# Kernel tuning notes

Measured on AMD Instinct MI355X. Metric: run time of the kernel, lower is better.

The kernel has to match this reference:

```python
import jax, jax.numpy as jnp
import numpy as np

D_MODEL = 2048
NUM_HEADS = 16
HEAD_DIM = D_MODEL // NUM_HEADS


def setup_inputs() -> dict:
    key = jax.random.key(0)
    ks = jax.random.split(key, 9)
    B, S, D = 2, 2048, D_MODEL
    scale = 1.0 / np.sqrt(D)
    x = jax.random.normal(ks[0], (B, S, D), dtype=jnp.float32)
    # torch nn.Linear weights are [out, in]; y = x @ W.T + b
    wq = jax.random.normal(ks[1], (D, D), dtype=jnp.float32) * scale
    wk = jax.random.normal(ks[2], (D, D), dtype=jnp.float32) * scale
    wv = jax.random.normal(ks[3], (D, D), dtype=jnp.float32) * scale
    wo = jax.random.normal(ks[4], (D, D), dtype=jnp.float32) * scale
    bq = jax.random.normal(ks[5], (D,), dtype=jnp.float32) * scale
    bk = jax.random.normal(ks[6], (D,), dtype=jnp.float32) * scale
    bv = jax.random.normal(ks[7], (D,), dtype=jnp.float32) * scale
    bo = jax.random.normal(ks[8], (D,), dtype=jnp.float32) * scale
    return {"x": x, "wq": wq, "bq": bq, "wk": wk, "bk": bk,
            "wv": wv, "bv": bv, "wo": wo, "bo": bo}


def reference(x, wq, bq, wk, bk, wv, bv, wo, bo):
    B, S, D = x.shape
    H, Dh = NUM_HEADS, HEAD_DIM
    # projections (torch Linear: x @ W.T + b), reshape to [B, H, S, Dh]
    q = (x @ wq.T + bq).reshape(B, S, H, Dh).transpose(0, 2, 1, 3)
    k = (x @ wk.T + bk).reshape(B, S, H, Dh).transpose(0, 2, 1, 3)
    v = (x @ wv.T + bv).reshape(B, S, H, Dh).transpose(0, 2, 1, 3)
    scores = jnp.einsum("bhqd,bhkd->bhqk", q, k) / jnp.sqrt(jnp.float32(Dh))
    attn = jax.nn.softmax(scores, axis=-1)
    out = jnp.einsum("bhqk,bhkd->bhqd", attn, v)  # [B, H, S, Dh]
    out = out.transpose(0, 2, 1, 3).reshape(B, S, D)
    return out @ wo.T + bo
```

## Files before the change

kernel.cpp:

```cpp
#include <hip/hip_runtime.h>

#define DEV __device__ __forceinline__

typedef __attribute__((ext_vector_type(8))) short bf16x8;
typedef __attribute__((ext_vector_type(4))) float f32x4;

constexpr int D_MODEL = 2048;
constexpr int NHEAD = 16;
constexpr int DH = 128;
constexpr int SS = 2048;
constexpr int KK = 2048;

DEV unsigned short f2bf(float f) {
  unsigned int u = __builtin_bit_cast(unsigned int, f);
  u = (u + 0x7fff + ((u >> 16) & 1)) >> 16;
  return (unsigned short)u;
}

DEV void async16(const void* g, void* l) {
  __builtin_amdgcn_global_load_lds(
      (const __attribute__((address_space(1))) unsigned int*)g,
      (__attribute__((address_space(3))) unsigned int*)l, 16, 0, 0);
}

DEV f32x4 mfma16(bf16x8 a, bf16x8 b, f32x4 c) {
  return __builtin_amdgcn_mfma_f32_16x16x32_bf16(a, b, c, 0, 0, 0);
}

__global__ __launch_bounds__(256) void cast_all(
    const float* __restrict__ x, const float* __restrict__ wq,
    const float* __restrict__ wk, const float* __restrict__ wv,
    const float* __restrict__ wo, unsigned short* __restrict__ xb,
    unsigned short* __restrict__ wb) {
  long i4 = ((long)blockIdx.x * 256 + threadIdx.x) * 4;
  const float* src;
  unsigned short* dst;
  long off;
  if (i4 < 8388608) {
    src = x; dst = xb; off = i4;
  } else {
    long j = i4 - 8388608;
    int seg = (int)(j >> 22);
    off = j & 4194303;
    src = (seg == 0) ? wq : (seg == 1) ? wk : (seg == 2) ? wv : wo;
    dst = wb + ((long)seg << 22);
  }
  float4 v = *(const float4*)(src + off);
  ushort4 u;
  u.x = f2bf(v.x); u.y = f2bf(v.y); u.z = f2bf(v.z); u.w = f2bf(v.w);
  *(ushort4*)(dst + off) = u;
}

template <int MODE>
__global__ __launch_bounds__(256, 2) void gemm_bt(
    const unsigned short* __restrict__ A, const unsigned short* __restrict__ W,
    const float* __restrict__ b0, const float* __restrict__ b1,
    const float* __restrict__ b2, unsigned short* __restrict__ oq,
    unsigned short* __restrict__ ok, unsigned short* __restrict__ ov,
    float* __restrict__ of) {
  __shared__ unsigned short lA[128 * 32];
  __shared__ unsigned short lB[128 * 32];
  const int t = threadIdx.x;
  const int lane = t & 63, wid = t >> 6;
  const int m0 = blockIdx.y * 128, n0 = blockIdx.x * 128;
  const int srow = t >> 2, scol = (t & 3) * 8;
  const unsigned short* ga = A + (long)(m0 + srow) * KK + scol;
  const unsigned short* gw = W + (long)(n0 + srow) * KK + scol;
  const int i16 = lane & 15, g4 = lane >> 4;
  const int wr = wid >> 1, wc = wid & 1;
  f32x4 acc[4][4] = {};
  for (int k0 = 0; k0 < KK; k0 += 32) {
    async16(ga + k0, &lA[wid * 512]);
    async16(ga + 64 * KK + k0, &lA[2048 + wid * 512]);
    async16(gw + k0, &lB[wid * 512]);
    async16(gw + 64 * KK + k0, &lB[2048 + wid * 512]);
    __syncthreads();
    bf16x8 af[4], bfr[4];
#pragma unroll
    for (int i = 0; i < 4; i++)
      af[i] = *(const bf16x8*)&lA[(wr * 64 + i * 16 + i16) * 32 + g4 * 8];
#pragma unroll
    for (int j = 0; j < 4; j++)
      bfr[j] = *(const bf16x8*)&lB[(wc * 64 + j * 16 + i16) * 32 + g4 * 8];
#pragma unroll
    for (int i = 0; i < 4; i++)
#pragma unroll
      for (int j = 0; j < 4; j++) acc[i][j] = mfma16(af[i], bfr[j], acc[i][j]);
    __syncthreads();
  }
#pragma unroll
  for (int i = 0; i < 4; i++) {
#pragma unroll
    for (int j = 0; j < 4; j++) {
      const int ng = n0 + wc * 64 + j * 16 + i16;
#pragma unroll
      for (int r = 0; r < 4; r++) {
        const int mg = m0 + wr * 64 + i * 16 + g4 * 4 + r;
        float v = acc[i][j][r];
        if (MODE == 1) {
          v += b0[ng];
          of[(long)mg * D_MODEL + ng] = v;
        } else {
          const int seg = ng >> 11, n = ng & 2047;
          const int h = n >> 7, d = n & 127;
          const int b_ = mg >> 11, s_ = mg & 2047;
          const long bh = b_ * NHEAD + h;
          if (seg == 0) {
            v = (v + b0[n]) * 0.08838834764831845f;
            oq[(bh * SS + s_) * DH + d] = f2bf(v);
          } else if (seg == 1) {
            v += b1[n];
            ok[(bh * SS + s_) * DH + d] = f2bf(v);
          } else {
            v += b2[n];
            ov[(bh * DH + d) * SS + s_] = f2bf(v);
          }
        }
      }
    }
  }
}

__global__ __launch_bounds__(256, 2) void attn_fwd(
    const unsigned short* __restrict__ Q, const unsigned short* __restrict__ Kb,
    const unsigned short* __restrict__ Vt, unsigned short* __restrict__ Ob) {
  __shared__ unsigned short lK[64 * 128];
  __shared__ unsigned short lV[128 * 64];
  __shared__ unsigned short lP[4][16 * 64];
  const int t = threadIdx.x, lane = t & 63, wid = t >> 6;
  const int i16 = lane & 15, g4 = lane >> 4;
  const int qt = blockIdx.x, bh = blockIdx.y;
  const long qrow = (long)bh * SS + qt * 64 + wid * 16 + i16;
  bf16x8 qa[4];
#pragma unroll
  for (int ks = 0; ks < 4; ks++)
    qa[ks] = *(const bf16x8*)&Q[qrow * DH + ks * 32 + g4 * 8];
  f32x4 o[8] = {};
  float mrow[4] = {-1e30f, -1e30f, -1e30f, -1e30f};
  float lrow[4] = {0.f, 0.f, 0.f, 0.f};
  const char* kbase = (const char*)(Kb + (long)bh * SS * DH);
  const char* vbase = (const char*)(Vt + (long)bh * DH * SS);
  for (int kv0 = 0; kv0 < SS; kv0 += 64) {
    bf16x8 kreg[4], vreg[4];
#pragma unroll
    for (int r = 0; r < 4; r++) {
      const int idx = r * 4096 + t * 16;
      kreg[r] = *(const bf16x8*)(kbase + (long)kv0 * 256 + idx);
      const int vrow = idx >> 7, vcol = idx & 127;
      vreg[r] = *(const bf16x8*)(vbase + (long)vrow * (SS * 2) + kv0 * 2 + vcol);
    }
#pragma unroll
    for (int r = 0; r < 4; r++) {
      const int idx = r * 4096 + t * 16;
      const int krow = idx >> 8, kcol = idx & 255;
      *(bf16x8*)((char*)lK + krow * 256 + (kcol ^ ((krow & 7) << 4))) = kreg[r];
      const int vrow = idx >> 7, vcol = idx & 127;
      *(bf16x8*)((char*)lV + vrow * 128 + (vcol ^ ((vrow & 7) << 4))) = vreg[r];
    }
    __syncthreads();
    f32x4 s4[4] = {};
#pragma unroll
    for (int kc = 0; kc < 4; kc++) {
      const int row = kc * 16 + i16;
#pragma unroll
      for (int ks = 0; ks < 4; ks++) {
        const int lb = row * 256 + ((ks * 64 + g4 * 16) ^ ((row & 7) << 4));
        bf16x8 kf = *(const bf16x8*)((const char*)lK + lb);
        s4[kc] = mfma16(qa[ks], kf, s4[kc]);
      }
    }
    float fac[4];
#pragma unroll
    for (int r = 0; r < 4; r++) {
      float mx = fmaxf(fmaxf(s4[0][r], s4[1][r]), fmaxf(s4[2][r], s4[3][r]));
      mx = fmaxf(mx, __shfl_xor(mx, 1));
      mx = fmaxf(mx, __shfl_xor(mx, 2));
      mx = fmaxf(mx, __shfl_xor(mx, 4));
      mx = fmaxf(mx, __shfl_xor(mx, 8));
      const float mnew = fmaxf(mrow[r], mx);
      fac[r] = __expf(mrow[r] - mnew);
      mrow[r] = mnew;
#pragma unroll
      for (int kc = 0; kc < 4; kc++) s4[kc][r] = __expf(s4[kc][r] - mnew);
      float su = s4[0][r] + s4[1][r] + s4[2][r] + s4[3][r];
      su += __shfl_xor(su, 1);
      su += __shfl_xor(su, 2);
      su += __shfl_xor(su, 4);
      su += __shfl_xor(su, 8);
      lrow[r] = lrow[r] * fac[r] + su;
    }
#pragma unroll
    for (int r = 0; r < 4; r++) {
      const int prow = g4 * 4 + r;
      const int swz = (prow & 7) << 4;
#pragma unroll
      for (int kc = 0; kc < 4; kc++) {
        const int col = kc * 16 + i16;
        *(unsigned short*)((char*)&lP[wid][0] + prow * 128 + ((col * 2) ^ swz)) =
            f2bf(s4[kc][r]);
      }
    }
#pragma unroll
    for (int df = 0; df < 8; df++)
#pragma unroll
      for (int r = 0; r < 4; r++) o[df][r] *= fac[r];
    bf16x8 pa[2];
#pragma unroll
    for (int ks = 0; ks < 2; ks++) {
      const int lb = i16 * 128 + ((ks * 64 + g4 * 16) ^ ((i16 & 7) << 4));
      pa[ks] = *(const bf16x8*)((const char*)&lP[wid][0] + lb);
    }
#pragma unroll
    for (int df = 0; df < 8; df++) {
#pragma unroll
      for (int ks = 0; ks < 2; ks++) {
        const int row = df * 16 + i16;
        const int lb = row * 128 + ((ks * 64 + g4 * 16) ^ ((row & 7) << 4));
        bf16x8 vf = *(const bf16x8*)((const char*)lV + lb);
        o[df] = mfma16(pa[ks], vf, o[df]);
      }
    }
    __syncthreads();
  }
  const int b_ = bh >> 4, h = bh & 15;
#pragma unroll
  for (int df = 0; df < 8; df++) {
#pragma unroll
    for (int r = 0; r < 4; r++) {
      const float v = o[df][r] / lrow[r];
      const long mg = (long)b_ * SS + qt * 64 + wid * 16 + g4 * 4 + r;
      Ob[mg * D_MODEL + h * DH + df * 16 + i16] = f2bf(v);
    }
  }
}

extern "C" void kernel_launch(void* const* d_in, const int* in_sizes, int n_in,
                              void* d_out, int out_size, void* d_ws,
                              size_t ws_size, hipStream_t stream) {
  const float* x = (const float*)d_in[0];
  const float* wq = (const float*)d_in[1];
  const float* bq = (const float*)d_in[2];
  const float* wk = (const float*)d_in[3];
  const float* bk = (const float*)d_in[4];
  const float* wv = (const float*)d_in[5];
  const float* bv = (const float*)d_in[6];
  const float* wo = (const float*)d_in[7];
  const float* bo = (const float*)d_in[8];
  char* ws = (char*)d_ws;
  unsigned short* xb = (unsigned short*)(ws);
  unsigned short* wb = (unsigned short*)(ws + (16l << 20));
  unsigned short* wob = (unsigned short*)(ws + (40l << 20));
  unsigned short* Qb = (unsigned short*)(ws + (48l << 20));
  unsigned short* Kbf = (unsigned short*)(ws + (64l << 20));
  unsigned short* Vtb = (unsigned short*)(ws + (80l << 20));
  unsigned short* Atb = (unsigned short*)(ws);

  cast_all<<<24576, 256, 0, stream>>>(x, wq, wk, wv, wo, xb, wb);
  gemm_bt<0><<<dim3(48, 32), 256, 0, stream>>>(xb, wb, bq, bk, bv, Qb, Kbf,
                                               Vtb, nullptr);
  attn_fwd<<<dim3(32, 32), 256, 0, stream>>>(Qb, Kbf, Vtb, Atb);
  gemm_bt<1><<<dim3(16, 32), 256, 0, stream>>>(
      Atb, wob, bo, nullptr, nullptr, nullptr, nullptr, nullptr,
      (float*)d_out);
}
```

Baseline: 523.4 us.

## Double-buffer K/V with async LDS loads and process two query tiles per wave

The attention kernel now stages K and V tiles straight into LDS with global_load_lds into two buffers, prefetching the next tile while the current one is computed. Each wave handles 32 query rows instead of 16, so every K/V fragment read from LDS feeds two MFMAs, and the grid is halved. MFMA sections are wrapped in s_setprio raises. The aim is to hide global load latency and cut LDS traffic per FLOP, at the cost of doubled LDS use and more registers, which may lower occupancy.

Measured after the change: 470.4 us. -10.1%, faster.

```diff
diff --git a/kernel.cpp b/kernel.cpp
--- a/kernel.cpp
+++ b/kernel.cpp
@@ -124,112 +124,143 @@
 __global__ __launch_bounds__(256, 2) void attn_fwd(
     const unsigned short* __restrict__ Q, const unsigned short* __restrict__ Kb,
     const unsigned short* __restrict__ Vt, unsigned short* __restrict__ Ob) {
-  __shared__ unsigned short lK[64 * 128];
-  __shared__ unsigned short lV[128 * 64];
+  __shared__ unsigned short lK[2][64 * 128];
+  __shared__ unsigned short lV[2][128 * 64];
   __shared__ unsigned short lP[4][16 * 64];
   const int t = threadIdx.x, lane = t & 63, wid = t >> 6;
   const int i16 = lane & 15, g4 = lane >> 4;
   const int qt = blockIdx.x, bh = blockIdx.y;
-  const long qrow = (long)bh * SS + qt * 64 + wid * 16 + i16;
-  bf16x8 qa[4];
-#pragma unroll
-  for (int ks = 0; ks < 4; ks++)
-    qa[ks] = *(const bf16x8*)&Q[qrow * DH + ks * 32 + g4 * 8];
-  f32x4 o[8] = {};
-  float mrow[4] = {-1e30f, -1e30f, -1e30f, -1e30f};
-  float lrow[4] = {0.f, 0.f, 0.f, 0.f};
+  bf16x8 qa[2][4];
+#pragma unroll
+  for (int qi = 0; qi < 2; qi++) {
+    const long qrow = (long)bh * SS + qt * 128 + wid * 32 + qi * 16 + i16;
+#pragma unroll
+    for (int ks = 0; ks < 4; ks++)
+      qa[qi][ks] = *(const bf16x8*)&Q[qrow * DH + ks * 32 + g4 * 8];
+  }
+  f32x4 o[2][8] = {};
+  float mrow[2][4] = {{-1e30f, -1e30f, -1e30f, -1e30f},
+                      {-1e30f, -1e30f, -1e30f, -1e30f}};
+  float lrow[2][4] = {};
   const char* kbase = (const char*)(Kb + (long)bh * SS * DH);
   const char* vbase = (const char*)(Vt + (long)bh * DH * SS);
-  for (int kv0 = 0; kv0 < SS; kv0 += 64) {
-    bf16x8 kreg[4], vreg[4];
+
+  auto STAGE = [&](int buf, int kv0) {
 #pragma unroll
     for (int r = 0; r < 4; r++) {
-      const int idx = r * 4096 + t * 16;
-      kreg[r] = *(const bf16x8*)(kbase + (long)kv0 * 256 + idx);
-      const int vrow = idx >> 7, vcol = idx & 127;
-      vreg[r] = *(const bf16x8*)(vbase + (long)vrow * (SS * 2) + kv0 * 2 + vcol);
-    }
-#pragma unroll
-    for (int r = 0; r < 4; r++) {
-      const int idx = r * 4096 + t * 16;
-      const int krow = idx >> 8, kcol = idx & 255;
-      *(bf16x8*)((char*)lK + krow * 256 + (kcol ^ ((krow & 7) << 4))) = kreg[r];
-      const int vrow = idx >> 7, vcol = idx & 127;
-      *(bf16x8*)((char*)lV + vrow * 128 + (vcol ^ ((vrow & 7) << 4))) = vreg[r];
-    }
-    __syncthreads();
-    f32x4 s4[4] = {};
+      const int o_ = r * 4096 + t * 16;
+      const int okk = o_ ^ (((o_ >> 8) & 7) << 4);
+      async16(kbase + (long)kv0 * 256 + okk,
+              (char*)lK + buf * 16384 + r * 4096 + wid * 1024);
+      const int vrow = o_ >> 7;
+      const int inr = (o_ ^ ((vrow & 7) << 4)) & 127;
+      async16(vbase + (long)vrow * (SS * 2) + kv0 * 2 + inr,
+              (char*)lV + buf * 16384 + r * 4096 + wid * 1024);
+    }
+  };
+
+  STAGE(0, 0);
+  asm volatile("s_waitcnt vmcnt(0)");
+  __syncthreads();
+  int cur = 0;
+  for (int it = 0; it < SS / 64; ++it) {
+    if (it + 1 < SS / 64) STAGE(cur ^ 1, (it + 1) * 64);
+    const char* kb = (const char*)lK + cur * 16384;
+    const char* vb = (const char*)lV + cur * 16384;
+    f32x4 s4[2][4] = {};
+    __builtin_amdgcn_s_setprio(1);
 #pragma unroll
     for (int kc = 0; kc < 4; kc++) {
       const int row = kc * 16 + i16;
 #pragma unroll
       for (int ks = 0; ks < 4; ks++) {
         const int lb = row * 256 + ((ks * 64 + g4 * 16) ^ ((row & 7) << 4));
-        bf16x8 kf = *(const bf16x8*)((const char*)lK + lb);
-        s4[kc] = mfma16(qa[ks], kf, s4[kc]);
-      }
-    }
-    float fac[4];
-#pragma unroll
-    for (int r = 0; r < 4; r++) {
-      float mx = fmaxf(fmaxf(s4[0][r], s4[1][r]), fmaxf(s4[2][r], s4[3][r]));
-      mx = fmaxf(mx, __shfl_xor(mx, 1));
-      mx = fmaxf(mx, __shfl_xor(mx, 2));
-      mx = fmaxf(mx, __shfl_xor(mx, 4));
-      mx = fmaxf(mx, __shfl_xor(mx, 8));
-      const float mnew = fmaxf(mrow[r], mx);
-      fac[r] = __expf(mrow[r] - mnew);
-      mrow[r] = mnew;
-#pragma unroll
-      for (int kc = 0; kc < 4; kc++) s4[kc][r] = __expf(s4[kc][r] - mnew);
-      float su = s4[0][r] + s4[1][r] + s4[2][r] + s4[3][r];
-      su += __shfl_xor(su, 1);
-      su += __shfl_xor(su, 2);
-      su += __shfl_xor(su, 4);
-      su += __shfl_xor(su, 8);
-      lrow[r] = lrow[r] * fac[r] + su;
-    }
-#pragma unroll
-    for (int r = 0; r < 4; r++) {
-      const int prow = g4 * 4 + r;
-      const int swz = (prow & 7) << 4;
-#pragma unroll
-      for (int kc = 0; kc < 4; kc++) {
-        const int col = kc * 16 + i16;
-        *(unsigned short*)((char*)&lP[wid][0] + prow * 128 + ((col * 2) ^ swz)) =
-            f2bf(s4[kc][r]);
-      }
-    }
-#pragma unroll
-    for (int df = 0; df < 8; df++)
-#pragma unroll
-      for (int r = 0; r < 4; r++) o[df][r] *= fac[r];
-    bf16x8 pa[2];
-#pragma unroll
-    for (int ks = 0; ks < 2; ks++) {
-      const int lb = i16 * 128 + ((ks * 64 + g4 * 16) ^ ((i16 & 7) << 4));
-      pa[ks] = *(const bf16x8*)((const char*)&lP[wid][0] + lb);
-    }
+        bf16x8 kf = *(const bf16x8*)(kb + lb);
+        s4[0][kc] = mfma16(qa[0][ks], kf, s4[0][kc]);
+        s4[1][kc] = mfma16(qa[1][ks], kf, s4[1][kc]);
+      }
+    }
+    __builtin_amdgcn_s_setprio(0);
+    float fac[2][4];
+#pragma unroll
+    for (int qi = 0; qi < 2; qi++) {
+#pragma unroll
+      for (int r = 0; r < 4; r++) {
+        float mx = fmaxf(fmaxf(s4[qi][0][r], s4[qi][1][r]),
+                         fmaxf(s4[qi][2][r], s4[qi][3][r]));
+        mx = fmaxf(mx, __shfl_xor(mx, 1));
+        mx = fmaxf(mx, __shfl_xor(mx, 2));
+        mx = fmaxf(mx, __shfl_xor(mx, 4));
+        mx = fmaxf(mx, __shfl_xor(mx, 8));
+        const float mnew = fmaxf(mrow[qi][r], mx);
+        fac[qi][r] = __expf(mrow[qi][r] - mnew);
+        mrow[qi][r] = mnew;
+#pragma unroll
+        for (int kc = 0; kc < 4; kc++)
+          s4[qi][kc][r] = __expf(s4[qi][kc][r] - mnew);
+        float su = s4[qi][0][r] + s4[qi][1][r] + s4[qi][2][r] + s4[qi][3][r];
+        su += __shfl_xor(su, 1);
+        su += __shfl_xor(su, 2);
+        su += __shfl_xor(su, 4);
+        su += __shfl_xor(su, 8);
+        lrow[qi][r] = lrow[qi][r] * fac[qi][r] + su;
+      }
+    }
+    bf16x8 pa[2][2];
+#pragma unroll
+    for (int qi = 0; qi < 2; qi++) {
+#pragma unroll
+      for (int r = 0; r < 4; r++) {
+        const int prow = g4 * 4 + r;
+        const int swz = (prow & 7) << 4;
+#pragma unroll
+        for (int kc = 0; kc < 4; kc++) {
+          const int col = kc * 16 + i16;
+          *(unsigned short*)((char*)&lP[wid][0] + prow * 128 +
+                             ((col * 2) ^ swz)) = f2bf(s4[qi][kc][r]);
+        }
+      }
+#pragma unroll
+      for (int ks = 0; ks < 2; ks++) {
+        const int lb = i16 * 128 + ((ks * 64 + g4 * 16) ^ ((i16 & 7) << 4));
+        pa[qi][ks] = *(const bf16x8*)((const char*)&lP[wid][0] + lb);
+      }
+    }
+#pragma unroll
+    for (int qi = 0; qi < 2; qi++)
+#pragma unroll
+      for (int df = 0; df < 8; df++)
+#pragma unroll
+        for (int r = 0; r < 4; r++) o[qi][df][r] *= fac[qi][r];
+    __builtin_amdgcn_s_setprio(1);
 #pragma unroll
     for (int df = 0; df < 8; df++) {
 #pragma unroll
       for (int ks = 0; ks < 2; ks++) {
         const int row = df * 16 + i16;
         const int lb = row * 128 + ((ks * 64 + g4 * 16) ^ ((row & 7) << 4));
-        bf16x8 vf = *(const bf16x8*)((const char*)lV + lb);
-        o[df] = mfma16(pa[ks], vf, o[df]);
-      }
-    }
+        bf16x8 vf = *(const bf16x8*)(vb + lb);
+        o[0][df] = mfma16(pa[0][ks], vf, o[0][df]);
+        o[1][df] = mfma16(pa[1][ks], vf, o[1][df]);
+      }
+    }
+    __builtin_amdgcn_s_setprio(0);
+    asm volatile("s_waitcnt vmcnt(0)");
     __syncthreads();
+    cur ^= 1;
   }
   const int b_ = bh >> 4, h = bh & 15;
 #pragma unroll
-  for (int df = 0; df < 8; df++) {
-#pragma unroll
-    for (int r = 0; r < 4; r++) {
-      const float v = o[df][r] / lrow[r];
-      const long mg = (long)b_ * SS + qt * 64 + wid * 16 + g4 * 4 + r;
-      Ob[mg * D_MODEL + h * DH + df * 16 + i16] = f2bf(v);
+  for (int qi = 0; qi < 2; qi++) {
+#pragma unroll
+    for (int df = 0; df < 8; df++) {
+#pragma unroll
+      for (int r = 0; r < 4; r++) {
+        const float v = o[qi][df][r] / lrow[qi][r];
+        const long mg =
+            (long)b_ * SS + qt * 128 + wid * 32 + qi * 16 + g4 * 4 + r;
+        Ob[mg * D_MODEL + h * DH + df * 16 + i16] = f2bf(v);
+      }
     }
   }
 }
@@ -258,7 +289,7 @@
   cast_all<<<24576, 256, 0, stream>>>(x, wq, wk, wv, wo, xb, wb);
   gemm_bt<0><<<dim3(48, 32), 256, 0, stream>>>(xb, wb, bq, bk, bv, Qb, Kbf,
                                                Vtb, nullptr);
-  attn_fwd<<<dim3(32, 32), 256, 0, stream>>>(Qb, Kbf, Vtb, Atb);
+  attn_fwd<<<dim3(16, 32), 256, 0, stream>>>(Qb, Kbf, Vtb, Atb);
   gemm_bt<1><<<dim3(16, 32), 256, 0, stream>>>(
       Atb, wob, bo, nullptr, nullptr, nullptr, nullptr, nullptr,
       (float*)d_out);
```
